# Optimization experiments

Hardware: AMD Instinct MI355X
Metric: run time of the kernel (lower is better)

## Reference

```python
import jax, jax.numpy as jnp
import numpy as np

N_HEADS = 16
DIMS = 1024
HEAD_SIZE = DIMS // N_HEADS


def setup_inputs() -> dict:
    key = jax.random.key(0)
    k1, k2, k3, k4, k5 = jax.random.split(key, 5)
    x = jax.random.normal(k1, (1, 4096, DIMS), dtype=jnp.float32)
    s = 1.0 / np.sqrt(DIMS)
    w_qkv = jax.random.uniform(k2, (3 * DIMS, DIMS), jnp.float32, -s, s)
    b_qkv = jax.random.uniform(k3, (3 * DIMS,), jnp.float32, -s, s)
    w_o = jax.random.uniform(k4, (DIMS, DIMS), jnp.float32, -s, s)
    b_o = jax.random.uniform(k5, (DIMS,), jnp.float32, -s, s)
    return {"x": x, "w_qkv": w_qkv, "b_qkv": b_qkv, "w_o": w_o, "b_o": b_o,
            "causal_mask": 1}


def reference(x, w_qkv, b_qkv, w_o, b_o, causal_mask):
    B, S, D = x.shape
    qkv = x @ w_qkv.T + b_qkv                      # [B,S,3D]
    q, k, v = jnp.split(qkv, 3, axis=-1)
    def heads(t):
        return t.reshape(B, S, N_HEADS, HEAD_SIZE).transpose(0, 2, 1, 3)  # [B,H,S,hd]
    q, k, v = heads(q), heads(k), heads(v)
    scores = jnp.einsum("bhsd,bhtd->bhst", q, k)   # [B,H,S,S]
    if causal_mask:
        tri = jnp.triu(jnp.ones((S, S), dtype=bool), k=1)
        scores = jnp.where(tri, -jnp.inf, scores)  # mask BEFORE scale, as in torch code
    scores = scores / np.sqrt(HEAD_SIZE)
    weights = jax.nn.softmax(scores, axis=-1)
    out = jnp.einsum("bhst,bhtd->bhsd", weights, v)  # [B,H,S,hd]
    out = out.transpose(0, 2, 1, 3).reshape(B, S, D)
    return out @ w_o.T + b_o
```

## Files before the change

### kernel.cpp

```cpp
#include <hip/hip_runtime.h>
#include <hip/hip_bf16.h>
#include <stdint.h>

typedef __attribute__((ext_vector_type(8))) short short8;
typedef __attribute__((ext_vector_type(4))) float f32x4;
typedef __attribute__((ext_vector_type(16))) float f32x16;
typedef __hip_bfloat16 bf16;

#define S_LEN 4096
#define DMODEL 1024
#define NH 16
#define HD 64
#define QSCALE 0.1803368801111f

static __device__ inline uint2 pack4(float4 v) {
  union { uint2 u; bf16 h[4]; } p;
  p.h[0] = (bf16)v.x; p.h[1] = (bf16)v.y; p.h[2] = (bf16)v.z; p.h[3] = (bf16)v.w;
  return p.u;
}

static __device__ inline uint32_t pack2(float a, float b) {
  union { uint32_t u; bf16 h[2]; } p;
  p.h[0] = (bf16)a; p.h[1] = (bf16)b;
  return p.u;
}

static __device__ inline void gload_lds16(const bf16* g, bf16* l) {
  __builtin_amdgcn_global_load_lds(
      (const __attribute__((address_space(1))) unsigned int*)g,
      (__attribute__((address_space(3))) unsigned int*)l, 16, 0, 0);
}

static __device__ inline int rot_idx(int r, int c) {
  return r * 64 + ((c + ((r & 7) << 3)) & 63);
}

__global__ __launch_bounds__(256)
void cvt_all(const float* __restrict__ x, const float* __restrict__ wq,
             const float* __restrict__ wo, bf16* __restrict__ xb,
             bf16* __restrict__ wqb, bf16* __restrict__ wob) {
  const int nx = S_LEN * DMODEL;
  const int nq = 3 * DMODEL * DMODEL;
  const int no = DMODEL * DMODEL;
  int i = (blockIdx.x * 256 + threadIdx.x) * 4;
  if (i < nx) {
    *(uint2*)(xb + i) = pack4(*(const float4*)(x + i));
  } else if (i < nx + nq) {
    int j = i - nx;
    *(uint2*)(wqb + j) = pack4(*(const float4*)(wq + j));
  } else if (i < nx + nq + no) {
    int j = i - nx - nq;
    *(uint2*)(wob + j) = pack4(*(const float4*)(wo + j));
  }
}

__global__ __launch_bounds__(256)
void gemm_qkv(const bf16* __restrict__ A, const bf16* __restrict__ B,
              const float* __restrict__ bias, bf16* __restrict__ qkv2,
              bf16* __restrict__ vt) {
  const int K = DMODEL;
  __shared__ bf16 sA[128 * 64];
  __shared__ bf16 sB[128 * 64];
  const int tid  = threadIdx.x;
  const int lane = tid & 63;
  const int wave = tid >> 6;
  const int wm = wave >> 1, wn = wave & 1;
  const int tileM = blockIdx.y * 128;
  const int tileN = blockIdx.x * 128;

  const int lrow = lane & 15;
  const int quad = lane >> 4;
  const int kq   = quad * 8;

  f32x4 acc[4][4];
#pragma unroll
  for (int i = 0; i < 4; i++)
#pragma unroll
    for (int j = 0; j < 4; j++) acc[i][j] = (f32x4){0.f, 0.f, 0.f, 0.f};

  const int trl = lane >> 3;
  const int cgl = (((lane & 7) - trl) & 7) << 3;
  const bf16* aP[4];
  const bf16* bP[4];
#pragma unroll
  for (int c = 0; c < 4; c++) {
    int ch = wave * 4 + c;
    aP[c] = A + (size_t)(tileM + ch * 8 + trl) * K + cgl;
    bP[c] = B + (size_t)(tileN + ch * 8 + trl) * K + cgl;
  }

  for (int k0 = 0; k0 < K; k0 += 64) {
    __syncthreads();
#pragma unroll
    for (int c = 0; c < 4; c++) {
      int ch = wave * 4 + c;
      gload_lds16(aP[c] + k0, sA + ch * 512);
      gload_lds16(bP[c] + k0, sB + ch * 512);
    }
    __syncthreads();
#pragma unroll
    for (int ks = 0; ks < 2; ks++) {
      short8 afrag[4], bfrag[4];
#pragma unroll
      for (int mi = 0; mi < 4; mi++)
        afrag[mi] = *(const short8*)(sA + rot_idx(wm * 64 + mi * 16 + lrow, ks * 32 + kq));
#pragma unroll
      for (int ni = 0; ni < 4; ni++)
        bfrag[ni] = *(const short8*)(sB + rot_idx(wn * 64 + ni * 16 + lrow, ks * 32 + kq));
#pragma unroll
      for (int mi = 0; mi < 4; mi++)
#pragma unroll
        for (int ni = 0; ni < 4; ni++)
          acc[mi][ni] = __builtin_amdgcn_mfma_f32_16x16x32_bf16(afrag[mi], bfrag[ni], acc[mi][ni], 0, 0, 0);
    }
  }

#pragma unroll
  for (int ni = 0; ni < 4; ni++) {
    int col = tileN + wn * 64 + ni * 16 + lrow;
    float bv = bias[col];
    if (col < 2 * DMODEL) {
      float sc = (col < DMODEL) ? QSCALE : 1.0f;
#pragma unroll
      for (int mi = 0; mi < 4; mi++) {
        int row0 = tileM + wm * 64 + mi * 16 + quad * 4;
#pragma unroll
        for (int r = 0; r < 4; r++)
          qkv2[(size_t)(row0 + r) * 2048 + col] = (bf16)((acc[mi][ni][r] + bv) * sc);
      }
    } else {
      int cc = col - 2 * DMODEL;
      int hh = cc >> 6, dd = cc & 63;
      bf16* vrow = vt + ((size_t)(hh * 64 + dd)) * S_LEN;
#pragma unroll
      for (int mi = 0; mi < 4; mi++) {
        int row0 = tileM + wm * 64 + mi * 16 + quad * 4;
        float4 v = {acc[mi][ni][0] + bv, acc[mi][ni][1] + bv,
                    acc[mi][ni][2] + bv, acc[mi][ni][3] + bv};
        *(uint2*)(vrow + row0) = pack4(v);
      }
    }
  }
}

__global__ __launch_bounds__(256)
void gemm_oproj(const bf16* __restrict__ A, const bf16* __restrict__ B,
                const float* __restrict__ bias, float* __restrict__ C) {
  const int K = DMODEL, N = DMODEL;
  __shared__ bf16 sA[128 * 64];
  __shared__ bf16 sB[64 * 64];
  const int tid  = threadIdx.x;
  const int lane = tid & 63;
  const int wave = tid >> 6;
  const int wm = wave >> 1, wn = wave & 1;
  const int tileM = blockIdx.y * 128;
  const int tileN = blockIdx.x * 64;

  const int lrow = lane & 15;
  const int quad = lane >> 4;
  const int kq   = quad * 8;

  f32x4 acc[4][2];
#pragma unroll
  for (int i = 0; i < 4; i++)
#pragma unroll
    for (int j = 0; j < 2; j++) acc[i][j] = (f32x4){0.f, 0.f, 0.f, 0.f};

  const int trl = lane >> 3;
  const int cgl = (((lane & 7) - trl) & 7) << 3;
  const bf16* aP[4];
  const bf16* bP[2];
#pragma unroll
  for (int c = 0; c < 4; c++) {
    int ch = wave * 4 + c;
    aP[c] = A + (size_t)(tileM + ch * 8 + trl) * K + cgl;
  }
#pragma unroll
  for (int c = 0; c < 2; c++) {
    int ch = wave * 2 + c;
    bP[c] = B + (size_t)(tileN + ch * 8 + trl) * K + cgl;
  }

  for (int k0 = 0; k0 < K; k0 += 64) {
    __syncthreads();
#pragma unroll
    for (int c = 0; c < 4; c++)
      gload_lds16(aP[c] + k0, sA + (wave * 4 + c) * 512);
#pragma unroll
    for (int c = 0; c < 2; c++)
      gload_lds16(bP[c] + k0, sB + (wave * 2 + c) * 512);
    __syncthreads();
#pragma unroll
    for (int ks = 0; ks < 2; ks++) {
      short8 afrag[4], bfrag[2];
#pragma unroll
      for (int mi = 0; mi < 4; mi++)
        afrag[mi] = *(const short8*)(sA + rot_idx(wm * 64 + mi * 16 + lrow, ks * 32 + kq));
#pragma unroll
      for (int ni = 0; ni < 2; ni++)
        bfrag[ni] = *(const short8*)(sB + rot_idx(wn * 32 + ni * 16 + lrow, ks * 32 + kq));
#pragma unroll
      for (int mi = 0; mi < 4; mi++)
#pragma unroll
        for (int ni = 0; ni < 2; ni++)
          acc[mi][ni] = __builtin_amdgcn_mfma_f32_16x16x32_bf16(afrag[mi], bfrag[ni], acc[mi][ni], 0, 0, 0);
    }
  }

#pragma unroll
  for (int ni = 0; ni < 2; ni++) {
    int col = tileN + wn * 32 + ni * 16 + lrow;
    float bv = bias[col];
#pragma unroll
    for (int mi = 0; mi < 4; mi++) {
      int row0 = tileM + wm * 64 + mi * 16 + quad * 4;
#pragma unroll
      for (int r = 0; r < 4; r++)
        C[(size_t)(row0 + r) * N + col] = acc[mi][ni][r] + bv;
    }
  }
}

__global__ __launch_bounds__(256)
void gemm_qkv_f32(const float* __restrict__ A, const float* __restrict__ B,
                  const float* __restrict__ bias, bf16* __restrict__ qkv2,
                  bf16* __restrict__ vt) {
  const int K = DMODEL;
  __shared__ bf16 sA[128 * 64];
  __shared__ bf16 sB[128 * 64];
  const int tid  = threadIdx.x;
  const int lane = tid & 63;
  const int wave = tid >> 6;
  const int wm = wave >> 1, wn = wave & 1;
  const int tileM = blockIdx.y * 128;
  const int tileN = blockIdx.x * 128;
  const int lrow = lane & 15;
  const int quad = lane >> 4;
  const int kq   = quad * 8;

  f32x4 acc[4][4];
#pragma unroll
  for (int i = 0; i < 4; i++)
#pragma unroll
    for (int j = 0; j < 4; j++) acc[i][j] = (f32x4){0.f, 0.f, 0.f, 0.f};

  const int r0 = tid >> 4;
  const int cc = (tid & 15) * 4;

  for (int k0 = 0; k0 < K; k0 += 64) {
    uint2 ra[8], rb[8];
#pragma unroll
    for (int i = 0; i < 8; i++) {
      int row = r0 + i * 16;
      ra[i] = pack4(*(const float4*)(A + (size_t)(tileM + row) * K + k0 + cc));
      rb[i] = pack4(*(const float4*)(B + (size_t)(tileN + row) * K + k0 + cc));
    }
    __syncthreads();
#pragma unroll
    for (int i = 0; i < 8; i++) {
      int row = r0 + i * 16;
      *(uint2*)(sA + row * 64 + cc) = ra[i];
      *(uint2*)(sB + row * 64 + cc) = rb[i];
    }
    __syncthreads();
#pragma unroll
    for (int ks = 0; ks < 2; ks++) {
      short8 afrag[4], bfrag[4];
#pragma unroll
      for (int mi = 0; mi < 4; mi++)
        afrag[mi] = *(const short8*)(sA + (wm * 64 + mi * 16 + lrow) * 64 + ks * 32 + kq);
#pragma unroll
      for (int ni = 0; ni < 4; ni++)
        bfrag[ni] = *(const short8*)(sB + (wn * 64 + ni * 16 + lrow) * 64 + ks * 32 + kq);
#pragma unroll
      for (int mi = 0; mi < 4; mi++)
#pragma unroll
        for (int ni = 0; ni < 4; ni++)
          acc[mi][ni] = __builtin_amdgcn_mfma_f32_16x16x32_bf16(afrag[mi], bfrag[ni], acc[mi][ni], 0, 0, 0);
    }
  }
#pragma unroll
  for (int ni = 0; ni < 4; ni++) {
    int col = tileN + wn * 64 + ni * 16 + lrow;
    float bv = bias[col];
    if (col < 2 * DMODEL) {
      float sc = (col < DMODEL) ? QSCALE : 1.0f;
#pragma unroll
      for (int mi = 0; mi < 4; mi++) {
        int row0 = tileM + wm * 64 + mi * 16 + quad * 4;
#pragma unroll
        for (int r = 0; r < 4; r++)
          qkv2[(size_t)(row0 + r) * 2048 + col] = (bf16)((acc[mi][ni][r] + bv) * sc);
      }
    } else {
      int c2 = col - 2 * DMODEL;
      int hh = c2 >> 6, dd = c2 & 63;
      bf16* vrow = vt + ((size_t)(hh * 64 + dd)) * S_LEN;
#pragma unroll
      for (int mi = 0; mi < 4; mi++) {
        int row0 = tileM + wm * 64 + mi * 16 + quad * 4;
        float4 v = {acc[mi][ni][0] + bv, acc[mi][ni][1] + bv,
                    acc[mi][ni][2] + bv, acc[mi][ni][3] + bv};
        *(uint2*)(vrow + row0) = pack4(v);
      }
    }
  }
}

__global__ __launch_bounds__(256)
void gemm_oproj_f32w(const bf16* __restrict__ A, const float* __restrict__ B,
                     const float* __restrict__ bias, float* __restrict__ C) {
  const int K = DMODEL, N = DMODEL;
  __shared__ bf16 sA[128 * 64];
  __shared__ bf16 sB[128 * 64];
  const int tid  = threadIdx.x;
  const int lane = tid & 63;
  const int wave = tid >> 6;
  const int wm = wave >> 1, wn = wave & 1;
  const int tileM = blockIdx.y * 128;
  const int tileN = blockIdx.x * 128;
  const int lrow = lane & 15;
  const int quad = lane >> 4;
  const int kq   = quad * 8;

  f32x4 acc[4][4];
#pragma unroll
  for (int i = 0; i < 4; i++)
#pragma unroll
    for (int j = 0; j < 4; j++) acc[i][j] = (f32x4){0.f, 0.f, 0.f, 0.f};

  const int a_r0 = tid >> 3;
  const int a_cc = (tid & 7) * 8;
  const int b_r0 = tid >> 4;
  const int b_cc = (tid & 15) * 4;

  for (int k0 = 0; k0 < K; k0 += 64) {
    uint4 ra[4];
    uint2 rb[8];
#pragma unroll
    for (int i = 0; i < 4; i++)
      ra[i] = *(const uint4*)(A + (size_t)(tileM + a_r0 + i * 32) * K + k0 + a_cc);
#pragma unroll
    for (int i = 0; i < 8; i++)
      rb[i] = pack4(*(const float4*)(B + (size_t)(tileN + b_r0 + i * 16) * K + k0 + b_cc));
    __syncthreads();
#pragma unroll
    for (int i = 0; i < 4; i++)
      *(uint4*)(sA + (a_r0 + i * 32) * 64 + a_cc) = ra[i];
#pragma unroll
    for (int i = 0; i < 8; i++)
      *(uint2*)(sB + (b_r0 + i * 16) * 64 + b_cc) = rb[i];
    __syncthreads();
#pragma unroll
    for (int ks = 0; ks < 2; ks++) {
      short8 afrag[4], bfrag[4];
#pragma unroll
      for (int mi = 0; mi < 4; mi++)
        afrag[mi] = *(const short8*)(sA + (wm * 64 + mi * 16 + lrow) * 64 + ks * 32 + kq);
#pragma unroll
      for (int ni = 0; ni < 4; ni++)
        bfrag[ni] = *(const short8*)(sB + (wn * 64 + ni * 16 + lrow) * 64 + ks * 32 + kq);
#pragma unroll
      for (int mi = 0; mi < 4; mi++)
#pragma unroll
        for (int ni = 0; ni < 4; ni++)
          acc[mi][ni] = __builtin_amdgcn_mfma_f32_16x16x32_bf16(afrag[mi], bfrag[ni], acc[mi][ni], 0, 0, 0);
    }
  }
#pragma unroll
  for (int ni = 0; ni < 4; ni++) {
    int col = tileN + wn * 64 + ni * 16 + lrow;
    float bv = bias[col];
#pragma unroll
    for (int mi = 0; mi < 4; mi++) {
      int row0 = tileM + wm * 64 + mi * 16 + quad * 4;
#pragma unroll
      for (int r = 0; r < 4; r++)
        C[(size_t)(row0 + r) * N + col] = acc[mi][ni][r] + bv;
    }
  }
}

__global__ __launch_bounds__(256, 2)
void attn_kernel(const bf16* __restrict__ qkv2, const bf16* __restrict__ vt,
                 bf16* __restrict__ attn_out, const int* __restrict__ causal_ptr) {
  __shared__ bf16 sQ[128 * 64];
  __shared__ bf16 sK[2][64 * 64];
  __shared__ bf16 sV[2][64 * 64];

  const int tid  = threadIdx.x;
  const int lane = tid & 63;
  const int wave = tid >> 6;
  const int h  = blockIdx.y;
  const int qi = (h < 8) ? (int)blockIdx.x : (31 - (int)blockIdx.x);
  const int qbase = qi * 128;
  const bool causal = (*causal_ptr) != 0;

  const int l31 = lane & 31;
  const int hi  = lane >> 5;

  const int trl = lane >> 3;
  const int cgl = (((lane & 7) - trl) & 7) << 3;

  const bf16* Qb = qkv2 + h * HD;
  const bf16* Kb = qkv2 + DMODEL + h * HD;
  const bf16* Vb = vt + (size_t)(h * HD) * S_LEN;

#pragma unroll
  for (int i = 0; i < 4; i++) {
    int ch = wave * 4 + i;
    gload_lds16(Qb + (size_t)(qbase + ch * 8 + trl) * 2048 + cgl, sQ + ch * 512);
  }
#pragma unroll
  for (int i = 0; i < 2; i++) {
    int ch = wave * 2 + i;
    int trow = ch * 8 + trl;
    gload_lds16(Kb + (size_t)trow * 2048 + cgl, sK[0] + ch * 512);
    gload_lds16(Vb + (size_t)trow * S_LEN + cgl, sV[0] + ch * 512);
  }

  f32x16 oacc[2];
#pragma unroll
  for (int nc = 0; nc < 2; nc++)
#pragma unroll
    for (int e = 0; e < 16; e++) oacc[nc][e] = 0.f;
  float l_st = 0.f;

  const int nkt = causal ? (2 * qi + 2) : (S_LEN / 64);
  const int wrmin = qbase + wave * 32;
  const int wrmax = wrmin + 31;
  const int q_g   = wrmin + l31;

  __syncthreads();
  short8 qf[4];
#pragma unroll
  for (int kd = 0; kd < 4; kd++)
    qf[kd] = *(const short8*)(sQ + rot_idx(wave * 32 + l31, kd * 16 + hi * 8));

  for (int jt = 0; jt < nkt; jt++) {
    const int cur = jt & 1;
    const int kbase = jt * 64;
    __syncthreads();

    if (jt + 1 < nkt) {
      const int kb2 = kbase + 64;
#pragma unroll
      for (int i = 0; i < 2; i++) {
        int ch = wave * 2 + i;
        int trow = ch * 8 + trl;
        gload_lds16(Kb + (size_t)(kb2 + trow) * 2048 + cgl, sK[cur ^ 1] + ch * 512);
        gload_lds16(Vb + (size_t)trow * S_LEN + kb2 + cgl, sV[cur ^ 1] + ch * 512);
      }
    }
    if (causal && kbase > wrmax) continue;

    uint32_t pw[4][4];
#pragma unroll
    for (int kc = 0; kc < 2; kc++) {
      if (causal && (kbase + kc * 32 > wrmax)) {
#pragma unroll
        for (int w = 0; w < 4; w++) { pw[kc * 2][w] = 0u; pw[kc * 2 + 1][w] = 0u; }
      } else {
        f32x16 sacc;
#pragma unroll
        for (int e = 0; e < 16; e++) sacc[e] = 0.f;
#pragma unroll
        for (int kd = 0; kd < 4; kd++) {
          short8 kf = *(const short8*)(sK[cur] + rot_idx(kc * 32 + l31, kd * 16 + hi * 8));
          sacc = __builtin_amdgcn_mfma_f32_32x32x16_bf16(kf, qf[kd], sacc, 0, 0, 0);
        }
        const bool nm = causal && (kbase + kc * 32 + 31 > wrmin);
        float p[16];
        float psum = 0.f;
#pragma unroll
        for (int g = 0; g < 4; g++) {
#pragma unroll
          for (int r = 0; r < 4; r++) {
            float v = __builtin_amdgcn_exp2f(sacc[g * 4 + r]);
            if (nm) {
              int kg = kbase + kc * 32 + g * 8 + hi * 4 + r;
              if (kg > q_g) v = 0.f;
            }
            p[g * 4 + r] = v;
            psum += v;
          }
        }
        l_st += psum;
        uint32_t pku[4][2];
#pragma unroll
        for (int g = 0; g < 4; g++) {
#pragma unroll
          for (int h2 = 0; h2 < 2; h2++)
            pku[g][h2] = pack2(p[g * 4 + h2 * 2], p[g * 4 + h2 * 2 + 1]);
        }
#pragma unroll
        for (int c2 = 0; c2 < 2; c2++) {
#pragma unroll
          for (int h2 = 0; h2 < 2; h2++) {
            uint32_t a = pku[2 * c2][h2], b = pku[2 * c2 + 1][h2];
            uint32_t sa = (uint32_t)__shfl_xor((int)a, 32);
            uint32_t sb = (uint32_t)__shfl_xor((int)b, 32);
            pw[kc * 2 + c2][h2]     = hi ? sb : a;
            pw[kc * 2 + c2][2 + h2] = hi ? b  : sa;
          }
        }
      }
    }

#pragma unroll
    for (int kk = 0; kk < 4; kk++) {
      if (causal && (kbase + kk * 16 > wrmax)) continue;
      union { short8 s; uint32_t u[4]; } pf;
#pragma unroll
      for (int w = 0; w < 4; w++) pf.u[w] = pw[kk][w];
#pragma unroll
      for (int nc = 0; nc < 2; nc++) {
        short8 vf = *(const short8*)(sV[cur] + rot_idx(nc * 32 + l31, kk * 16 + hi * 8));
        oacc[nc] = __builtin_amdgcn_mfma_f32_32x32x16_bf16(pf.s, vf, oacc[nc], 0, 0, 0);
      }
    }
  }

  float ltot = l_st + __shfl_xor(l_st, 32);
  float* l_lds = (float*)sQ;
  if (hi == 0) l_lds[wave * 32 + l31] = ltot;
  float invl[4][4];
#pragma unroll
  for (int g = 0; g < 4; g++) {
    f32x4 lv = *(const f32x4*)(l_lds + wave * 32 + g * 8 + hi * 4);
#pragma unroll
    for (int r = 0; r < 4; r++) invl[g][r] = 1.0f / fmaxf(lv[r], 1e-30f);
  }
#pragma unroll
  for (int nc = 0; nc < 2; nc++) {
#pragma unroll
    for (int g = 0; g < 4; g++) {
#pragma unroll
      for (int r = 0; r < 4; r++) {
        int qg = qbase + wave * 32 + g * 8 + hi * 4 + r;
        int col = h * HD + nc * 32 + l31;
        attn_out[(size_t)qg * DMODEL + col] = (bf16)(oacc[nc][g * 4 + r] * invl[g][r]);
      }
    }
  }
}

extern "C" void kernel_launch(void* const* d_in, const int* in_sizes, int n_in,
                              void* d_out, int out_size, void* d_ws, size_t ws_size,
                              hipStream_t stream) {
  const float* x     = (const float*)d_in[0];
  const float* w_qkv = (const float*)d_in[1];
  const float* b_qkv = (const float*)d_in[2];
  const float* w_o   = (const float*)d_in[3];
  const float* b_o   = (const float*)d_in[4];
  const int*   cm    = (const int*)d_in[5];

  char* ws = (char*)d_ws;
  bf16* qkv2 = (bf16*)ws;
  bf16* vt   = (bf16*)(ws + 16777216);
  bf16* attn = (bf16*)(ws + 25165824);
  bf16* xb   = (bf16*)(ws + 33554432);
  bf16* wqb  = (bf16*)(ws + 41943040);
  bf16* wob  = (bf16*)(ws + 48234496);

  dim3 blk(256);
  const bool fast = (ws_size >= (size_t)50331648);

  if (fast) {
    const int ntot = S_LEN * DMODEL + 3 * DMODEL * DMODEL + DMODEL * DMODEL;
    cvt_all<<<dim3((ntot / 4 + 255) / 256), blk, 0, stream>>>(
        x, w_qkv, w_o, xb, wqb, wob);
    gemm_qkv<<<dim3(3 * DMODEL / 128, S_LEN / 128), blk, 0, stream>>>(
        xb, wqb, b_qkv, qkv2, vt);
    attn_kernel<<<dim3(S_LEN / 128, NH), blk, 0, stream>>>(qkv2, vt, attn, cm);
    gemm_oproj<<<dim3(DMODEL / 64, S_LEN / 128), blk, 0, stream>>>(
        attn, wob, b_o, (float*)d_out);
  } else {
    gemm_qkv_f32<<<dim3(3 * DMODEL / 128, S_LEN / 128), blk, 0, stream>>>(
        x, w_qkv, b_qkv, qkv2, vt);
    attn_kernel<<<dim3(S_LEN / 128, NH), blk, 0, stream>>>(qkv2, vt, attn, cm);
    gemm_oproj_f32w<<<dim3(DMODEL / 128, S_LEN / 128), blk, 0, stream>>>(
        attn, w_o, b_o, (float*)d_out);
  }
}
```

Baseline: 256.1 us.

## Split attention KV tiles across wave pairs with smaller query blocks and XCD-aware mapping

```diff
diff --git a/kernel.cpp b/kernel.cpp
--- a/kernel.cpp
+++ b/kernel.cpp
@@ -5,6 +5,7 @@
 typedef __attribute__((ext_vector_type(8))) short short8;
 typedef __attribute__((ext_vector_type(4))) float f32x4;
 typedef __attribute__((ext_vector_type(16))) float f32x16;
+typedef __attribute__((ext_vector_type(2))) unsigned int uint2u;
 typedef __hip_bfloat16 bf16;
 
 #define S_LEN 4096
@@ -381,19 +382,27 @@
   }
 }
 
-__global__ __launch_bounds__(256, 2)
+__global__ __launch_bounds__(256, 4)
 void attn_kernel(const bf16* __restrict__ qkv2, const bf16* __restrict__ vt,
                  bf16* __restrict__ attn_out, const int* __restrict__ causal_ptr) {
-  __shared__ bf16 sQ[128 * 64];
+  __shared__ bf16 sQ[64 * 64];
   __shared__ bf16 sK[2][64 * 64];
   __shared__ bf16 sV[2][64 * 64];
 
   const int tid  = threadIdx.x;
   const int lane = tid & 63;
   const int wave = tid >> 6;
-  const int h  = blockIdx.y;
-  const int qi = (h < 8) ? (int)blockIdx.x : (31 - (int)blockIdx.x);
-  const int qbase = qi * 128;
+  const int qh   = wave >> 1;
+  const int kh   = wave & 1;
+
+  const int id  = blockIdx.y * 64 + blockIdx.x;
+  const int xcd = id & 7;
+  const int jj  = id >> 3;
+  const int hh  = jj >> 6;
+  const int h   = xcd + (hh << 3);
+  const int qw  = jj & 63;
+  const int qi  = hh ? (63 - qw) : qw;
+  const int qbase = qi * 64;
   const bool causal = (*causal_ptr) != 0;
 
   const int l31 = lane & 31;
@@ -407,8 +416,8 @@
   const bf16* Vb = vt + (size_t)(h * HD) * S_LEN;
 
 #pragma unroll
-  for (int i = 0; i < 4; i++) {
-    int ch = wave * 4 + i;
+  for (int i = 0; i < 2; i++) {
+    int ch = wave * 2 + i;
     gload_lds16(Qb + (size_t)(qbase + ch * 8 + trl) * 2048 + cgl, sQ + ch * 512);
   }
 #pragma unroll
@@ -426,8 +435,8 @@
     for (int e = 0; e < 16; e++) oacc[nc][e] = 0.f;
   float l_st = 0.f;
 
-  const int nkt = causal ? (2 * qi + 2) : (S_LEN / 64);
-  const int wrmin = qbase + wave * 32;
+  const int nkt = causal ? (qi + 1) : (S_LEN / 64);
+  const int wrmin = qbase + qh * 32;
   const int wrmax = wrmin + 31;
   const int q_g   = wrmin + l31;
 
@@ -435,7 +444,7 @@
   short8 qf[4];
 #pragma unroll
   for (int kd = 0; kd < 4; kd++)
-    qf[kd] = *(const short8*)(sQ + rot_idx(wave * 32 + l31, kd * 16 + hi * 8));
+    qf[kd] = *(const short8*)(sQ + rot_idx(qh * 32 + l31, kd * 16 + hi * 8));
 
   for (int jt = 0; jt < nkt; jt++) {
     const int cur = jt & 1;
@@ -452,94 +461,114 @@
         gload_lds16(Vb + (size_t)trow * S_LEN + kb2 + cgl, sV[cur ^ 1] + ch * 512);
       }
     }
-    if (causal && kbase > wrmax) continue;
-
-    uint32_t pw[4][4];
-#pragma unroll
-    for (int kc = 0; kc < 2; kc++) {
-      if (causal && (kbase + kc * 32 > wrmax)) {
-#pragma unroll
-        for (int w = 0; w < 4; w++) { pw[kc * 2][w] = 0u; pw[kc * 2 + 1][w] = 0u; }
-      } else {
-        f32x16 sacc;
-#pragma unroll
-        for (int e = 0; e < 16; e++) sacc[e] = 0.f;
-#pragma unroll
-        for (int kd = 0; kd < 4; kd++) {
-          short8 kf = *(const short8*)(sK[cur] + rot_idx(kc * 32 + l31, kd * 16 + hi * 8));
-          sacc = __builtin_amdgcn_mfma_f32_32x32x16_bf16(kf, qf[kd], sacc, 0, 0, 0);
+    const int kh32 = kbase + kh * 32;
+    if (causal && kh32 > wrmax) continue;
+
+    uint32_t pw[2][4];
+    {
+      f32x16 sacc;
+#pragma unroll
+      for (int e = 0; e < 16; e++) sacc[e] = 0.f;
+      __builtin_amdgcn_s_setprio(1);
+#pragma unroll
+      for (int kd = 0; kd < 4; kd++) {
+        short8 kf = *(const short8*)(sK[cur] + rot_idx(kh * 32 + l31, kd * 16 + hi * 8));
+        sacc = __builtin_amdgcn_mfma_f32_32x32x16_bf16(kf, qf[kd], sacc, 0, 0, 0);
+      }
+      __builtin_amdgcn_s_setprio(0);
+      const bool nm = causal && (kh32 + 31 > wrmin);
+      float p[16];
+      float psum = 0.f;
+#pragma unroll
+      for (int g = 0; g < 4; g++) {
+#pragma unroll
+        for (int r = 0; r < 4; r++) {
+          float v = __builtin_amdgcn_exp2f(sacc[g * 4 + r]);
+          if (nm) {
+            int kg = kh32 + g * 8 + hi * 4 + r;
+            if (kg > q_g) v = 0.f;
+          }
+          p[g * 4 + r] = v;
+          psum += v;
         }
-        const bool nm = causal && (kbase + kc * 32 + 31 > wrmin);
-        float p[16];
-        float psum = 0.f;
-#pragma unroll
-        for (int g = 0; g < 4; g++) {
-#pragma unroll
-          for (int r = 0; r < 4; r++) {
-            float v = __builtin_amdgcn_exp2f(sacc[g * 4 + r]);
-            if (nm) {
-              int kg = kbase + kc * 32 + g * 8 + hi * 4 + r;
-              if (kg > q_g) v = 0.f;
-            }
-            p[g * 4 + r] = v;
-            psum += v;
-          }
+      }
+      l_st += psum;
+      uint32_t pku[4][2];
+#pragma unroll
+      for (int g = 0; g < 4; g++) {
+#pragma unroll
+        for (int h2 = 0; h2 < 2; h2++)
+          pku[g][h2] = pack2(p[g * 4 + h2 * 2], p[g * 4 + h2 * 2 + 1]);
+      }
+#pragma unroll
+      for (int c2 = 0; c2 < 2; c2++) {
+#pragma unroll
+        for (int h2 = 0; h2 < 2; h2++) {
+          uint2u sw = __builtin_amdgcn_permlane32_swap(
+              pku[2 * c2][h2], pku[2 * c2 + 1][h2], false, false);
+          pw[c2][h2]     = sw[0];
+          pw[c2][2 + h2] = sw[1];
         }
-        l_st += psum;
-        uint32_t pku[4][2];
-#pragma unroll
-        for (int g = 0; g < 4; g++) {
-#pragma unroll
-          for (int h2 = 0; h2 < 2; h2++)
-            pku[g][h2] = pack2(p[g * 4 + h2 * 2], p[g * 4 + h2 * 2 + 1]);
+      }
+    }
+
+    __builtin_amdgcn_s_setprio(1);
+#pragma unroll
+    for (int c2 = 0; c2 < 2; c2++) {
+      if (causal && (kh32 + c2 * 16 > wrmax)) continue;
+      union { short8 s; uint32_t u[4]; } pf;
+#pragma unroll
+      for (int w = 0; w < 4; w++) pf.u[w] = pw[c2][w];
+#pragma unroll
+      for (int nc = 0; nc < 2; nc++) {
+        short8 vf = *(const short8*)(sV[cur] +
+            rot_idx(nc * 32 + l31, (kh * 2 + c2) * 16 + hi * 8));
+        oacc[nc] = __builtin_amdgcn_mfma_f32_32x32x16_bf16(pf.s, vf, oacc[nc], 0, 0, 0);
+      }
+    }
+    __builtin_amdgcn_s_setprio(0);
+  }
+
+  __syncthreads();
+  float ltot = l_st + __shfl_xor(l_st, 32);
+  float* obuf = (float*)sK;
+  float* lbuf = (float*)sV;
+  if (kh == 1) {
+    float* ob = obuf + qh * 2048;
+#pragma unroll
+    for (int nc = 0; nc < 2; nc++)
+#pragma unroll
+      for (int e = 0; e < 16; e++)
+        ob[(nc * 16 + e) * 64 + lane] = oacc[nc][e];
+    if (hi == 0) lbuf[qh * 32 + l31] = ltot;
+  }
+  __syncthreads();
+  if (kh == 0) {
+    float* ob = obuf + qh * 2048;
+#pragma unroll
+    for (int nc = 0; nc < 2; nc++)
+#pragma unroll
+      for (int e = 0; e < 16; e++)
+        oacc[nc][e] += ob[(nc * 16 + e) * 64 + lane];
+    ltot += lbuf[qh * 32 + l31];
+    if (hi == 0) lbuf[64 + qh * 32 + l31] = ltot;
+    float invl[4][4];
+#pragma unroll
+    for (int g = 0; g < 4; g++) {
+      f32x4 lv = *(const f32x4*)(lbuf + 64 + qh * 32 + g * 8 + hi * 4);
+#pragma unroll
+      for (int r = 0; r < 4; r++) invl[g][r] = 1.0f / fmaxf(lv[r], 1e-30f);
+    }
+#pragma unroll
+    for (int nc = 0; nc < 2; nc++) {
+#pragma unroll
+      for (int g = 0; g < 4; g++) {
+#pragma unroll
+        for (int r = 0; r < 4; r++) {
+          int qg = qbase + qh * 32 + g * 8 + hi * 4 + r;
+          int col = h * HD + nc * 32 + l31;
+          attn_out[(size_t)qg * DMODEL + col] = (bf16)(oacc[nc][g * 4 + r] * invl[g][r]);
         }
-#pragma unroll
-        for (int c2 = 0; c2 < 2; c2++) {
-#pragma unroll
-          for (int h2 = 0; h2 < 2; h2++) {
-            uint32_t a = pku[2 * c2][h2], b = pku[2 * c2 + 1][h2];
-            uint32_t sa = (uint32_t)__shfl_xor((int)a, 32);
-            uint32_t sb = (uint32_t)__shfl_xor((int)b, 32);
-            pw[kc * 2 + c2][h2]     = hi ? sb : a;
-            pw[kc * 2 + c2][2 + h2] = hi ? b  : sa;
-          }
-        }
-      }
-    }
-
-#pragma unroll
-    for (int kk = 0; kk < 4; kk++) {
-      if (causal && (kbase + kk * 16 > wrmax)) continue;
-      union { short8 s; uint32_t u[4]; } pf;
-#pragma unroll
-      for (int w = 0; w < 4; w++) pf.u[w] = pw[kk][w];
-#pragma unroll
-      for (int nc = 0; nc < 2; nc++) {
-        short8 vf = *(const short8*)(sV[cur] + rot_idx(nc * 32 + l31, kk * 16 + hi * 8));
-        oacc[nc] = __builtin_amdgcn_mfma_f32_32x32x16_bf16(pf.s, vf, oacc[nc], 0, 0, 0);
-      }
-    }
-  }
-
-  float ltot = l_st + __shfl_xor(l_st, 32);
-  float* l_lds = (float*)sQ;
-  if (hi == 0) l_lds[wave * 32 + l31] = ltot;
-  float invl[4][4];
-#pragma unroll
-  for (int g = 0; g < 4; g++) {
-    f32x4 lv = *(const f32x4*)(l_lds + wave * 32 + g * 8 + hi * 4);
-#pragma unroll
-    for (int r = 0; r < 4; r++) invl[g][r] = 1.0f / fmaxf(lv[r], 1e-30f);
-  }
-#pragma unroll
-  for (int nc = 0; nc < 2; nc++) {
-#pragma unroll
-    for (int g = 0; g < 4; g++) {
-#pragma unroll
-      for (int r = 0; r < 4; r++) {
-        int qg = qbase + wave * 32 + g * 8 + hi * 4 + r;
-        int col = h * HD + nc * 32 + l31;
-        attn_out[(size_t)qg * DMODEL + col] = (bf16)(oacc[nc][g * 4 + r] * invl[g][r]);
       }
     }
   }
@@ -572,13 +601,13 @@
         x, w_qkv, w_o, xb, wqb, wob);
     gemm_qkv<<<dim3(3 * DMODEL / 128, S_LEN / 128), blk, 0, stream>>>(
         xb, wqb, b_qkv, qkv2, vt);
-    attn_kernel<<<dim3(S_LEN / 128, NH), blk, 0, stream>>>(qkv2, vt, attn, cm);
+    attn_kernel<<<dim3(S_LEN / 64, NH), blk, 0, stream>>>(qkv2, vt, attn, cm);
     gemm_oproj<<<dim3(DMODEL / 64, S_LEN / 128), blk, 0, stream>>>(
         attn, wob, b_o, (float*)d_out);
   } else {
     gemm_qkv_f32<<<dim3(3 * DMODEL / 128, S_LEN / 128), blk, 0, stream>>>(
         x, w_qkv, b_qkv, qkv2, vt);
-    attn_kernel<<<dim3(S_LEN / 128, NH), blk, 0, stream>>>(qkv2, vt, attn, cm);
+    attn_kernel<<<dim3(S_LEN / 64, NH), blk, 0, stream>>>(qkv2, vt, attn, cm);
     gemm_oproj_f32w<<<dim3(DMODEL / 128, S_LEN / 128), blk, 0, stream>>>(
         attn, w_o, b_o, (float*)d_out);
   }
```

Measured after the change: 221.0 us. -13.7%, faster.
